# Optimization experiments

Measured on AMD Instinct MI355X. Metric: run time of the kernel, lower is better.

The kernel has to match this reference:

```python
import jax, jax.numpy as jnp
import numpy as np

N_HEADS = 16
D_HEAD = 64
MAX_POS = 128

def setup_inputs() -> dict:
    key = jax.random.key(0)
    ks = jax.random.split(key, 9)
    B, L, D = 4, 1024, 1024
    s = 0.02
    return {
        'x': jax.random.normal(ks[0], (B, L, D), jnp.float32),
        'pad_mask': jnp.ones((B, L), jnp.float32),
        'Wq': jax.random.normal(ks[1], (D, D), jnp.float32) * s,
        'bq': jnp.zeros((D,), jnp.float32),
        'Wk': jax.random.normal(ks[2], (D, D), jnp.float32) * s,
        'bk': jnp.zeros((D,), jnp.float32),
        'Wv': jax.random.normal(ks[3], (D, D), jnp.float32) * s,
        'bv': jnp.zeros((D,), jnp.float32),
        'Wo': jax.random.normal(ks[4], (D, D), jnp.float32) * s,
        'bo': jnp.zeros((D,), jnp.float32),
        'posK': jax.random.normal(ks[5], (2 * MAX_POS + 1, D_HEAD), jnp.float32) * s,
        'posV': jax.random.normal(ks[6], (2 * MAX_POS + 1, D_HEAD), jnp.float32) * s,
    }

def reference(x, pad_mask, Wq, bq, Wk, bk, Wv, bv, Wo, bo, posK, posV):
    B, L, _ = x.shape
    H, d = N_HEADS, D_HEAD
    def proj(W, b):
        y = x @ W + b                      # [B, L, H*d]
        return y.reshape(B, L, H, d).transpose(0, 2, 1, 3)  # [B, H, L, d]
    Q = proj(Wq, bq)
    K = proj(Wk, bk)
    V = proj(Wv, bv)
    # relative position index, clamped to [-MAX_POS, MAX_POS], shifted to [0, 2*MAX_POS]
    idx = jnp.arange(L)
    pos_index = jnp.clip(idx[None, :] - idx[:, None], -MAX_POS, MAX_POS) + MAX_POS  # [L, L]
    pos_emb_K = posK[pos_index]            # [L, L, d]
    pos_emb_V = posV[pos_index]            # [L, L, d]
    S1 = jnp.einsum('bhqd,bhkd->bhqk', Q, K)
    S2 = jnp.einsum('bhqd,qkd->bhqk', Q, pos_emb_K)
    S = (S1 + S2) / np.sqrt(d).astype(np.float32)
    # NOTE: original multiplies scores by the pad mask (not additive -inf)
    S = S * pad_mask[:, None, None, :]
    A = jax.nn.softmax(S, axis=-1)
    O1 = jnp.einsum('bhqk,bhkd->bhqd', A, V)
    O2 = jnp.einsum('bhqk,qkd->bhqd', A, pos_emb_V)
    out = (O1 + O2).transpose(0, 2, 1, 3).reshape(B, L, H * d)
    return out @ Wo + bo
```

## Files before the change

### kernel.cpp

```cpp
#include <hip/hip_runtime.h>
#include <math.h>

#define L_SEQ 1024
#define NB 4
#define NH 16
#define DH 64
#define BH_TOT (NB * NH)
#define GQ_TOT (BH_TOT * L_SEQ)
#define NPOS 257
#define QP_STRIDE 260
#define LDK 72
#define LDQP 68
#define LDPV 264

typedef unsigned short ushort_t;
typedef __attribute__((ext_vector_type(8))) short bf16x8;
typedef __attribute__((ext_vector_type(4))) float f32x4;

__device__ inline ushort_t f2bf_rne(float x) {
    unsigned u = __float_as_uint(x);
    unsigned r = u + 0x7FFFu + ((u >> 16) & 1u);
    return (ushort_t)(r >> 16);
}
__device__ inline float bf2f(ushort_t h) {
    return __uint_as_float(((unsigned)h) << 16);
}
__device__ inline void split8(float4 a0, float4 a1, uint4* H, uint4* L) {
    float v[8] = {a0.x, a0.y, a0.z, a0.w, a1.x, a1.y, a1.z, a1.w};
    unsigned hh[4], ll[4];
    #pragma unroll
    for (int j = 0; j < 4; j++) {
        ushort_t h0 = f2bf_rne(v[2*j]),   h1 = f2bf_rne(v[2*j+1]);
        ushort_t l0 = f2bf_rne(v[2*j]   - bf2f(h0));
        ushort_t l1 = f2bf_rne(v[2*j+1] - bf2f(h1));
        hh[j] = (unsigned)h0 | ((unsigned)h1 << 16);
        ll[j] = (unsigned)l0 | ((unsigned)l1 << 16);
    }
    *H = (uint4){hh[0], hh[1], hh[2], hh[3]};
    *L = (uint4){ll[0], ll[1], ll[2], ll[3]};
}
__device__ inline uint4 pack8hi(float4 a0, float4 a1) {
    float v[8] = {a0.x, a0.y, a0.z, a0.w, a1.x, a1.y, a1.z, a1.w};
    unsigned hh[4];
    #pragma unroll
    for (int j = 0; j < 4; j++)
        hh[j] = (unsigned)f2bf_rne(v[2*j]) | ((unsigned)f2bf_rne(v[2*j+1]) << 16);
    return (uint4){hh[0], hh[1], hh[2], hh[3]};
}

__global__ __launch_bounds__(256)
void split_f32(const float* __restrict__ A, ushort_t* __restrict__ hi,
               ushort_t* __restrict__ lo)
{
    const size_t base = ((size_t)blockIdx.x * 256 + threadIdx.x) * 8;
    uint4 H, L;
    split8(*(const float4*)(A + base), *(const float4*)(A + base + 4), &H, &L);
    *(uint4*)(hi + base) = H;
    *(uint4*)(lo + base) = L;
}

__global__ __launch_bounds__(256)
void split_transpose(const float* __restrict__ W, ushort_t* __restrict__ Thi,
                     ushort_t* __restrict__ Tlo, int Kdim, int Ndim)
{
    __shared__ float Ws[64][65];
    const int tid = threadIdx.x;
    const int k0 = blockIdx.x * 64;
    const int n0 = blockIdx.y * 64;
    const int r  = tid >> 4;
    const int c4 = (tid & 15) * 4;
    #pragma unroll
    for (int i = 0; i < 4; i++) {
        float4 v = *(const float4*)(W + (size_t)(k0 + r + i*16) * Ndim + n0 + c4);
        Ws[r + i*16][c4+0] = v.x;
        Ws[r + i*16][c4+1] = v.y;
        Ws[r + i*16][c4+2] = v.z;
        Ws[r + i*16][c4+3] = v.w;
    }
    __syncthreads();
    #pragma unroll
    for (int i = 0; i < 4; i++) {
        const int nl = r + i*16;
        ushort_t h[4], l[4];
        #pragma unroll
        for (int j = 0; j < 4; j++) {
            float x = Ws[c4 + j][nl];
            h[j] = f2bf_rne(x);
            l[j] = f2bf_rne(x - bf2f(h[j]));
        }
        size_t off = (size_t)(n0 + nl) * Kdim + k0 + c4;
        uint2 H, L;
        H.x = (unsigned)h[0] | ((unsigned)h[1] << 16);
        H.y = (unsigned)h[2] | ((unsigned)h[3] << 16);
        L.x = (unsigned)l[0] | ((unsigned)l[1] << 16);
        L.y = (unsigned)l[2] | ((unsigned)l[3] << 16);
        *(uint2*)(Thi + off) = H;
        *(uint2*)(Tlo + off) = L;
    }
}

__global__ __launch_bounds__(256)
void prep_pvt(const float* __restrict__ posV, ushort_t* __restrict__ pvTg)
{
    __shared__ float Ws[64][65];
    const int tid = threadIdx.x;
    const int c = blockIdx.x;
    {
        const int r  = tid >> 2;
        const int d0 = (tid & 3) * 16;
        const float* src = posV + (size_t)(c * 64 + r + 1) * 64 + d0;
        #pragma unroll
        for (int i = 0; i < 4; i++) {
            float4 v = *(const float4*)(src + i * 4);
            Ws[r][d0 + i*4 + 0] = v.x;
            Ws[r][d0 + i*4 + 1] = v.y;
            Ws[r][d0 + i*4 + 2] = v.z;
            Ws[r][d0 + i*4 + 3] = v.w;
        }
    }
    __syncthreads();
    {
        const int d  = tid >> 2;
        const int r0 = (tid & 3) * 16;
        #pragma unroll
        for (int k = 0; k < 16; k++)
            pvTg[(size_t)d * LDPV + c * 64 + r0 + k] = f2bf_rne(Ws[r0 + k][d]);
    }
}

__global__ __launch_bounds__(256)
void gemm_mfma(const ushort_t* __restrict__ Ahi, const ushort_t* __restrict__ Alo,
               const ushort_t* __restrict__ Bhi, const ushort_t* __restrict__ Blo,
               const float* __restrict__ bias, float* __restrict__ C,
               int M, int N, int K, int mode)
{
    __shared__ ushort_t As[2][64 * LDK];
    __shared__ ushort_t Bs[2][64 * LDK];
    const int tid  = threadIdx.x;
    const int m0   = blockIdx.x * 64;
    const int n0   = blockIdx.y * 64;
    const int wave = tid >> 6;
    const int lane = tid & 63;
    const int w0 = wave >> 1;
    const int w1 = wave & 1;
    const int lr = lane & 15;
    const int lq = lane >> 4;

    f32x4 acc[2][2];
    #pragma unroll
    for (int i = 0; i < 2; i++)
        #pragma unroll
        for (int j = 0; j < 2; j++)
            acc[i][j] = (f32x4){0.f, 0.f, 0.f, 0.f};

    for (int k0 = 0; k0 < K; k0 += 64) {
        __syncthreads();
        #pragma unroll
        for (int c = 0; c < 2; c++) {
            const int n   = c * 256 + tid;
            const int row = n >> 3;
            const int col = (n & 7) * 8;
            const size_t ga = (size_t)(m0 + row) * K + k0 + col;
            const size_t gb = (size_t)(n0 + row) * K + k0 + col;
            const int la = row * LDK + col;
            *(uint4*)&As[0][la] = *(const uint4*)(Ahi + ga);
            *(uint4*)&As[1][la] = *(const uint4*)(Alo + ga);
            *(uint4*)&Bs[0][la] = *(const uint4*)(Bhi + gb);
            *(uint4*)&Bs[1][la] = *(const uint4*)(Blo + gb);
        }
        __syncthreads();
        #pragma unroll
        for (int ks = 0; ks < 2; ks++) {
            bf16x8 ah[2], al[2], bh[2], bl[2];
            #pragma unroll
            for (int i = 0; i < 2; i++) {
                const int ar = (w0*32 + i*16 + lr) * LDK + ks*32 + lq*8;
                ah[i] = *(const bf16x8*)&As[0][ar];
                al[i] = *(const bf16x8*)&As[1][ar];
                const int br = (w1*32 + i*16 + lr) * LDK + ks*32 + lq*8;
                bh[i] = *(const bf16x8*)&Bs[0][br];
                bl[i] = *(const bf16x8*)&Bs[1][br];
            }
            #pragma unroll
            for (int i = 0; i < 2; i++)
                #pragma unroll
                for (int j = 0; j < 2; j++) {
                    acc[i][j] = __builtin_amdgcn_mfma_f32_16x16x32_bf16(ah[i], bh[j], acc[i][j], 0, 0, 0);
                    acc[i][j] = __builtin_amdgcn_mfma_f32_16x16x32_bf16(ah[i], bl[j], acc[i][j], 0, 0, 0);
                    acc[i][j] = __builtin_amdgcn_mfma_f32_16x16x32_bf16(al[i], bh[j], acc[i][j], 0, 0, 0);
                }
        }
    }

    #pragma unroll
    for (int j = 0; j < 2; j++) {
        const int colg = n0 + w1*32 + j*16 + lr;
        const float bcol = bias[colg];
        #pragma unroll
        for (int i = 0; i < 2; i++) {
            #pragma unroll
            for (int r = 0; r < 4; r++) {
                const int m = m0 + w0*32 + i*16 + lq*4 + r;
                const float v = acc[i][j][r] + bcol;
                if (mode == 0) {
                    C[(size_t)m * N + colg] = v;
                } else if (mode == 1) {
                    const int b = m >> 10, lp = m & 1023;
                    const int h = colg >> 6, dd = colg & 63;
                    C[((size_t)(b * NH + h) * L_SEQ + lp) * DH + dd] = v;
                } else {
                    const int b = m >> 10, lp = m & 1023;
                    const int h = colg >> 6, dd = colg & 63;
                    C[((size_t)(b * NH + h) * DH + dd) * L_SEQ + lp] = v;
                }
            }
        }
    }
}

__global__ __launch_bounds__(256)
void qp_kernel(const float* __restrict__ Q, const float* __restrict__ posK,
               ushort_t* __restrict__ Qpu)
{
    __shared__ float Qt[64 * 64];
    __shared__ float Pt[64 * 64];
    const int tid = threadIdx.x;
    const size_t gq0 = (size_t)blockIdx.x * 64;
    const int ty = tid >> 4;
    const int tx = tid & 15;

    {
        const int q  = tid >> 2;
        const int d0 = (tid & 3) * 16;
        const float* qrow = Q + (gq0 + q) * DH + d0;
        #pragma unroll
        for (int i = 0; i < 4; i++) {
            float4 v = *(const float4*)(qrow + i * 4);
            Qt[(d0 + i*4 + 0) * 64 + q] = v.x;
            Qt[(d0 + i*4 + 1) * 64 + q] = v.y;
            Qt[(d0 + i*4 + 2) * 64 + q] = v.z;
            Qt[(d0 + i*4 + 3) * 64 + q] = v.w;
        }
    }

    for (int c = 0; c < 4; c++) {
        __syncthreads();
        {
            const int r  = tid >> 2;
            const int d0 = (tid & 3) * 16;
            const float* krow = posK + (size_t)(c * 64 + r) * DH + d0;
            #pragma unroll
            for (int i = 0; i < 4; i++) {
                float4 v = *(const float4*)(krow + i * 4);
                Pt[(d0 + i*4 + 0) * 64 + r] = v.x;
                Pt[(d0 + i*4 + 1) * 64 + r] = v.y;
                Pt[(d0 + i*4 + 2) * 64 + r] = v.z;
                Pt[(d0 + i*4 + 3) * 64 + r] = v.w;
            }
        }
        __syncthreads();

        float acc[16];
        #pragma unroll
        for (int i = 0; i < 16; i++) acc[i] = 0.f;
        #pragma unroll 16
        for (int d = 0; d < 64; d++) {
            float4 qv = *(const float4*)&Qt[d * 64 + ty * 4];
            float4 pv = *(const float4*)&Pt[d * 64 + tx * 4];
            float qa[4] = {qv.x, qv.y, qv.z, qv.w};
            float pa[4] = {pv.x, pv.y, pv.z, pv.w};
            #pragma unroll
            for (int i = 0; i < 4; i++)
                #pragma unroll
                for (int j = 0; j < 4; j++)
                    acc[i * 4 + j] += qa[i] * pa[j];
        }
        #pragma unroll
        for (int i = 0; i < 4; i++) {
            uint2 o;
            o.x = (unsigned)f2bf_rne(acc[i*4+0]) | ((unsigned)f2bf_rne(acc[i*4+1]) << 16);
            o.y = (unsigned)f2bf_rne(acc[i*4+2]) | ((unsigned)f2bf_rne(acc[i*4+3]) << 16);
            *(uint2*)(Qpu + (gq0 + ty * 4 + i) * QP_STRIDE + c * 64 + tx * 4) = o;
        }
    }

    __syncthreads();
    if (tid < 64) {
        float s = 0.f;
        #pragma unroll 16
        for (int d = 0; d < 64; d++)
            s += Qt[d * 64 + tid] * posK[256 * 64 + d];
        Qpu[(gq0 + tid) * QP_STRIDE + 256] = f2bf_rne(s);
    }
}

__global__ __launch_bounds__(256)
void attn_kernel(const float* __restrict__ Q, const float* __restrict__ K,
                 const float* __restrict__ Vt, const ushort_t* __restrict__ Qpu,
                 const float* __restrict__ pm,
                 ushort_t* __restrict__ SbandU,
                 float* __restrict__ O1a, float* __restrict__ O1b,
                 float* __restrict__ lsum2, float* __restrict__ clo2,
                 float* __restrict__ chi2)
{
    __shared__ ushort_t Qs[64 * LDK];
    __shared__ ushort_t KsPs[64 * LDK];
    __shared__ ushort_t Vs[64 * LDK];
    __shared__ ushort_t Qps[64 * LDQP];
    __shared__ float mk[64];
    __shared__ float redl[128], redc[128], redh[128];

    const int tid = threadIdx.x;
    const int blk = blockIdx.x;
    const int bh  = blk >> 5;
    const int qb  = (blk >> 1) & 15;
    const int ks  = blk & 1;
    const int b   = bh >> 4;
    const int q0  = qb * 64;
    const size_t gq0 = (size_t)bh * L_SEQ + q0;
    const int wave = tid >> 6, lane = tid & 63;
    const int w0 = wave >> 1, w1 = wave & 1;
    const int lr = lane & 15, lq = lane >> 4;

    #pragma unroll
    for (int c = 0; c < 2; c++) {
        const int slot = c * 256 + tid;
        const int row = slot >> 3, col = (slot & 7) * 8;
        const float* src = Q + (gq0 + row) * DH + col;
        *(uint4*)&Qs[row * LDK + col] =
            pack8hi(*(const float4*)src, *(const float4*)(src + 4));
    }

    if (ks == 0 && tid < 64) {
        const int q = q0 + tid;
        ushort_t* bandRow = SbandU + (gq0 + tid) * 256;
        for (int j = 0; j < 127 - q; j++)    bandRow[j] = 0;
        for (int j = 254; j > 1150 - q; j--) bandRow[j] = 0;
        bandRow[255] = 0;
    }

    f32x4 Oacc[2][2];
    #pragma unroll
    for (int i = 0; i < 2; i++)
        #pragma unroll
        for (int j = 0; j < 2; j++)
            Oacc[i][j] = (f32x4){0.f, 0.f, 0.f, 0.f};
    float lpart[2][4] = {}, clpart[2][4] = {}, chpart[2][4] = {};

    const float* Kg  = K  + (size_t)bh * (L_SEQ * DH);
    const float* Vtg = Vt + (size_t)bh * (DH * L_SEQ);

    for (int t = 0; t < 8; t++) {
        const int kt = ks * 8 + t;
        const int k0 = kt * 64;
        __syncthreads();

        #pragma unroll
        for (int c = 0; c < 2; c++) {
            const int slot = c * 256 + tid;
            const int row = slot >> 3, col = (slot & 7) * 8;
            const int la = row * LDK + col;
            const float* ksrc = Kg + (size_t)(k0 + row) * DH + col;
            *(uint4*)&KsPs[la] =
                pack8hi(*(const float4*)ksrc, *(const float4*)(ksrc + 4));
            const float* vsrc = Vtg + (size_t)row * L_SEQ + k0 + col;
            *(uint4*)&Vs[la] =
                pack8hi(*(const float4*)vsrc, *(const float4*)(vsrc + 4));
        }
        #pragma unroll
        for (int tt = 0; tt < 16; tt++) {
            const int idx = tt * 256 + tid;
            const int ql = idx >> 6, kl = idx & 63;
            int rel = k0 + kl - q0 - ql;
            rel = rel < -128 ? -128 : (rel > 128 ? 128 : rel);
            Qps[ql * LDQP + kl] = Qpu[(gq0 + ql) * QP_STRIDE + rel + 128];
        }
        if (tid < 64) mk[tid] = pm[b * L_SEQ + k0 + tid];
        __syncthreads();

        f32x4 Sacc[2][2];
        #pragma unroll
        for (int i = 0; i < 2; i++)
            #pragma unroll
            for (int j = 0; j < 2; j++)
                Sacc[i][j] = (f32x4){0.f, 0.f, 0.f, 0.f};
        #pragma unroll
        for (int kc = 0; kc < 2; kc++) {
            bf16x8 ah[2], bhf[2];
            #pragma unroll
            for (int i = 0; i < 2; i++) {
                ah[i]  = *(const bf16x8*)&Qs[(w0*32 + i*16 + lr) * LDK + kc*32 + lq*8];
                bhf[i] = *(const bf16x8*)&KsPs[(w1*32 + i*16 + lr) * LDK + kc*32 + lq*8];
            }
            #pragma unroll
            for (int i = 0; i < 2; i++)
                #pragma unroll
                for (int j = 0; j < 2; j++)
                    Sacc[i][j] = __builtin_amdgcn_mfma_f32_16x16x32_bf16(ah[i], bhf[j], Sacc[i][j], 0, 0, 0);
        }

        ushort_t pb[2][2][4];
        #pragma unroll
        for (int i = 0; i < 2; i++) {
            #pragma unroll
            for (int r = 0; r < 4; r++) {
                const int ql = w0*32 + i*16 + lq*4 + r;
                const int q  = q0 + ql;
                const size_t gq = gq0 + ql;
                ushort_t* bandRow = SbandU + gq * 256 + 127;
                #pragma unroll
                for (int j = 0; j < 2; j++) {
                    const int kl = w1*32 + j*16 + lr;
                    const int k  = k0 + kl;
                    const int rel = k - q;
                    float s = (Sacc[i][j][r] + bf2f(Qps[ql * LDQP + kl])) * 0.125f;
                    s *= mk[kl];
                    const float p = __expf(s);
                    lpart[i][r] += p;
                    const ushort_t ph = f2bf_rne(p);
                    if (rel <= -128)      clpart[i][r] += p;
                    else if (rel >= 128)  chpart[i][r] += p;
                    else                  bandRow[rel] = ph;
                    pb[i][j][r] = ph;
                }
            }
        }
        __syncthreads();

        #pragma unroll
        for (int i = 0; i < 2; i++)
            #pragma unroll
            for (int j = 0; j < 2; j++)
                #pragma unroll
                for (int r = 0; r < 4; r++) {
                    const int ql = w0*32 + i*16 + lq*4 + r;
                    const int kl = w1*32 + j*16 + lr;
                    KsPs[ql * LDK + kl] = pb[i][j][r];
                }
        __syncthreads();

        #pragma unroll
        for (int kc = 0; kc < 2; kc++) {
            bf16x8 pa[2], vh[2];
            #pragma unroll
            for (int i = 0; i < 2; i++) {
                pa[i] = *(const bf16x8*)&KsPs[(w0*32 + i*16 + lr) * LDK + kc*32 + lq*8];
                vh[i] = *(const bf16x8*)&Vs[(w1*32 + i*16 + lr) * LDK + kc*32 + lq*8];
            }
            #pragma unroll
            for (int i = 0; i < 2; i++)
                #pragma unroll
                for (int j = 0; j < 2; j++)
                    Oacc[i][j] = __builtin_amdgcn_mfma_f32_16x16x32_bf16(pa[i], vh[j], Oacc[i][j], 0, 0, 0);
        }
    }

    #pragma unroll
    for (int off = 1; off < 16; off <<= 1) {
        #pragma unroll
        for (int i = 0; i < 2; i++)
            #pragma unroll
            for (int r = 0; r < 4; r++) {
                lpart[i][r]  += __shfl_xor(lpart[i][r],  off, 64);
                clpart[i][r] += __shfl_xor(clpart[i][r], off, 64);
                chpart[i][r] += __shfl_xor(chpart[i][r], off, 64);
            }
    }
    if (lr == 0) {
        #pragma unroll
        for (int i = 0; i < 2; i++)
            #pragma unroll
            for (int r = 0; r < 4; r++) {
                const int ql = w0*32 + i*16 + lq*4 + r;
                redl[w1 * 64 + ql] = lpart[i][r];
                redc[w1 * 64 + ql] = clpart[i][r];
                redh[w1 * 64 + ql] = chpart[i][r];
            }
    }
    __syncthreads();
    if (tid < 64) {
        const size_t o = (size_t)ks * GQ_TOT + gq0 + tid;
        lsum2[o] = redl[tid] + redl[64 + tid];
        clo2[o]  = redc[tid] + redc[64 + tid];
        chi2[o]  = redh[tid] + redh[64 + tid];
    }

    float* O1o = ks ? O1b : O1a;
    #pragma unroll
    for (int i = 0; i < 2; i++)
        #pragma unroll
        for (int j = 0; j < 2; j++)
            #pragma unroll
            for (int r = 0; r < 4; r++) {
                const int ql = w0*32 + i*16 + lq*4 + r;
                const int dd = w1*32 + j*16 + lr;
                O1o[(gq0 + ql) * DH + dd] = Oacc[i][j][r];
            }
}

__global__ __launch_bounds__(256)
void post_mfma(const ushort_t* __restrict__ SbandU, const ushort_t* __restrict__ pvTg,
               const float* __restrict__ O1a, const float* __restrict__ O1b,
               const float* __restrict__ lsum2, const float* __restrict__ clo2,
               const float* __restrict__ chi2, const float* __restrict__ posV,
               ushort_t* __restrict__ athi, ushort_t* __restrict__ atlo)
{
    __shared__ ushort_t pvT[64 * LDPV];
    const int tid = threadIdx.x;
    const size_t q0 = (size_t)blockIdx.x * 64;
    const int wave = tid >> 6, lane = tid & 63;
    const int w0 = wave >> 1, w1 = wave & 1;
    const int lr = lane & 15, lq = lane >> 4;

    {
        const unsigned* src = (const unsigned*)pvTg;
        unsigned* dst = (unsigned*)pvT;
        for (int i = tid; i < 64 * LDPV / 2; i += 256) dst[i] = src[i];
    }
    __syncthreads();

    f32x4 acc[2][2];
    #pragma unroll
    for (int i = 0; i < 2; i++)
        #pragma unroll
        for (int j = 0; j < 2; j++)
            acc[i][j] = (f32x4){0.f, 0.f, 0.f, 0.f};

    const ushort_t* bandB = SbandU + q0 * 256;
    #pragma unroll
    for (int kc = 0; kc < 8; kc++) {
        bf16x8 a[2], bv[2];
        #pragma unroll
        for (int i = 0; i < 2; i++) {
            a[i]  = *(const bf16x8*)&bandB[(size_t)(w0*32 + i*16 + lr) * 256 + kc*32 + lq*8];
            bv[i] = *(const bf16x8*)&pvT[(w1*32 + i*16 + lr) * LDPV + kc*32 + lq*8];
        }
        #pragma unroll
        for (int i = 0; i < 2; i++)
            #pragma unroll
            for (int j = 0; j < 2; j++)
                acc[i][j] = __builtin_amdgcn_mfma_f32_16x16x32_bf16(a[i], bv[j], acc[i][j], 0, 0, 0);
    }

    #pragma unroll
    for (int i = 0; i < 2; i++) {
        #pragma unroll
        for (int r = 0; r < 4; r++) {
            const int ql = w0*32 + i*16 + lq*4 + r;
            const size_t gq = q0 + ql;
            const float li = lsum2[gq] + lsum2[GQ_TOT + gq];
            const float cl = clo2[gq]  + clo2[GQ_TOT + gq];
            const float ch = chi2[gq]  + chi2[GQ_TOT + gq];
            const float inv = 1.0f / li;
            const int b  = (int)(gq >> 14);
            const int h  = (int)((gq >> 10) & 15);
            const int lp = (int)(gq & 1023);
            const size_t obase = ((size_t)(b * L_SEQ + lp) * 1024) + h * 64;
            #pragma unroll
            for (int j = 0; j < 2; j++) {
                const int dd = w1*32 + j*16 + lr;
                float o = O1a[gq * DH + dd] + O1b[gq * DH + dd] + acc[i][j][r]
                        + cl * posV[dd] + ch * posV[256 * 64 + dd];
                o *= inv;
                const ushort_t hh = f2bf_rne(o);
                const ushort_t ll = f2bf_rne(o - bf2f(hh));
                athi[obase + dd] = hh;
                atlo[obase + dd] = ll;
            }
        }
    }
}

extern "C" void kernel_launch(void* const* d_in, const int* in_sizes, int n_in,
                              void* d_out, int out_size, void* d_ws, size_t ws_size,
                              hipStream_t stream)
{
    const float* x    = (const float*)d_in[0];
    const float* pmk  = (const float*)d_in[1];
    const float* Wq   = (const float*)d_in[2];
    const float* bq   = (const float*)d_in[3];
    const float* Wk   = (const float*)d_in[4];
    const float* bk   = (const float*)d_in[5];
    const float* Wv   = (const float*)d_in[6];
    const float* bv   = (const float*)d_in[7];
    const float* Wo   = (const float*)d_in[8];
    const float* bo   = (const float*)d_in[9];
    const float* posK = (const float*)d_in[10];
    const float* posV = (const float*)d_in[11];
    float* out = (float*)d_out;

    float* ws = (float*)d_ws;
    float* Qb = ws;
    float* Kb = Qb + (size_t)GQ_TOT * DH;
    float* Vb = Kb + (size_t)GQ_TOT * DH;
    ushort_t* Qpu    = (ushort_t*)(Vb + (size_t)GQ_TOT * DH);
    ushort_t* SbandU = Qpu + (size_t)GQ_TOT * QP_STRIDE;
    ushort_t* athi   = SbandU + (size_t)GQ_TOT * 256;
    ushort_t* atlo   = athi + (size_t)GQ_TOT * DH;
    ushort_t* pvTg   = atlo + (size_t)GQ_TOT * DH;
    float* O1a   = (float*)(pvTg + 64 * LDPV);
    float* O1b   = O1a   + (size_t)GQ_TOT * DH;
    float* lsum2 = O1b   + (size_t)GQ_TOT * DH;
    float* clo2  = lsum2 + 2 * (size_t)GQ_TOT;
    float* chi2  = clo2  + 2 * (size_t)GQ_TOT;

    ushort_t* bb  = SbandU;
    ushort_t* xhi = bb;
    ushort_t* xlo = xhi + 4194304;
    ushort_t* wqh = xlo + 4194304;
    ushort_t* wql = wqh + 1048576;
    ushort_t* wkh = wql + 1048576;
    ushort_t* wkl = wkh + 1048576;
    ushort_t* wvh = wkl + 1048576;
    ushort_t* wvl = wvh + 1048576;
    ushort_t* woh = bb;
    ushort_t* wol = woh + 1048576;

    dim3 tg(16, 16), gg(64, 16), gb(256);

    split_f32<<<dim3(2048), gb, 0, stream>>>(x, xhi, xlo);
    split_transpose<<<tg, gb, 0, stream>>>(Wq, wqh, wql, 1024, 1024);
    split_transpose<<<tg, gb, 0, stream>>>(Wk, wkh, wkl, 1024, 1024);
    split_transpose<<<tg, gb, 0, stream>>>(Wv, wvh, wvl, 1024, 1024);
    prep_pvt<<<dim3(4), gb, 0, stream>>>(posV, pvTg);
    gemm_mfma<<<gg, gb, 0, stream>>>(xhi, xlo, wqh, wql, bq, Qb, 4096, 1024, 1024, 1);
    gemm_mfma<<<gg, gb, 0, stream>>>(xhi, xlo, wkh, wkl, bk, Kb, 4096, 1024, 1024, 1);
    gemm_mfma<<<gg, gb, 0, stream>>>(xhi, xlo, wvh, wvl, bv, Vb, 4096, 1024, 1024, 2);
    qp_kernel<<<dim3(GQ_TOT / 64), gb, 0, stream>>>(Qb, posK, Qpu);
    attn_kernel<<<dim3(2048), gb, 0, stream>>>(Qb, Kb, Vb, Qpu, pmk,
                                               SbandU, O1a, O1b, lsum2, clo2, chi2);
    post_mfma<<<dim3(GQ_TOT / 64), gb, 0, stream>>>(SbandU, pvTg, O1a, O1b, lsum2,
                                                    clo2, chi2, posV, athi, atlo);
    split_transpose<<<tg, gb, 0, stream>>>(Wo, woh, wol, 1024, 1024);
    gemm_mfma<<<gg, gb, 0, stream>>>(athi, atlo, woh, wol, bo, out, 4096, 1024, 1024, 0);
}
```

Baseline: 439.6 us.

## Restructure attention kernel: per-wave query rows, register Q, prefetch next K/V tile

```diff
diff --git a/kernel.cpp b/kernel.cpp
--- a/kernel.cpp
+++ b/kernel.cpp
@@ -10,7 +10,7 @@
 #define NPOS 257
 #define QP_STRIDE 260
 #define LDK 72
-#define LDQP 68
+#define LDQP 72
 #define LDPV 264
 
 typedef unsigned short ushort_t;
@@ -303,12 +303,10 @@
                  float* __restrict__ lsum2, float* __restrict__ clo2,
                  float* __restrict__ chi2)
 {
-    __shared__ ushort_t Qs[64 * LDK];
-    __shared__ ushort_t KsPs[64 * LDK];
+    __shared__ ushort_t Ks[64 * LDK];
     __shared__ ushort_t Vs[64 * LDK];
-    __shared__ ushort_t Qps[64 * LDQP];
+    __shared__ ushort_t QpsP[64 * LDQP];
     __shared__ float mk[64];
-    __shared__ float redl[128], redc[128], redh[128];
 
     const int tid = threadIdx.x;
     const int blk = blockIdx.x;
@@ -319,16 +317,26 @@
     const int q0  = qb * 64;
     const size_t gq0 = (size_t)bh * L_SEQ + q0;
     const int wave = tid >> 6, lane = tid & 63;
-    const int w0 = wave >> 1, w1 = wave & 1;
     const int lr = lane & 15, lq = lane >> 4;
-
-    #pragma unroll
-    for (int c = 0; c < 2; c++) {
-        const int slot = c * 256 + tid;
-        const int row = slot >> 3, col = (slot & 7) * 8;
-        const float* src = Q + (gq0 + row) * DH + col;
-        *(uint4*)&Qs[row * LDK + col] =
-            pack8hi(*(const float4*)src, *(const float4*)(src + 4));
+    const int qw = wave * 16;
+
+    const int sr0 = tid >> 3,          sc0 = (tid & 7) * 8;
+    const int sr1 = (256 + tid) >> 3,  sc1 = ((256 + tid) & 7) * 8;
+    const int qpRowL = qw + (lane >> 2);
+    const int qpCol0 = (lane & 3) * 16;
+
+    const float* Kg  = K  + (size_t)bh * (L_SEQ * DH);
+    const float* Vtg = Vt + (size_t)bh * (DH * L_SEQ);
+
+    bf16x8 qa[2];
+    {
+        const float* qrow = Q + (gq0 + qw + lr) * DH;
+        #pragma unroll
+        for (int kc = 0; kc < 2; kc++) {
+            const float* s = qrow + kc * 32 + lq * 8;
+            uint4 u = pack8hi(*(const float4*)s, *(const float4*)(s + 4));
+            qa[kc] = *(bf16x8*)&u;
+        }
     }
 
     if (ks == 0 && tid < 64) {
@@ -339,163 +347,149 @@
         bandRow[255] = 0;
     }
 
-    f32x4 Oacc[2][2];
-    #pragma unroll
-    for (int i = 0; i < 2; i++)
-        #pragma unroll
-        for (int j = 0; j < 2; j++)
-            Oacc[i][j] = (f32x4){0.f, 0.f, 0.f, 0.f};
-    float lpart[2][4] = {}, clpart[2][4] = {}, chpart[2][4] = {};
-
-    const float* Kg  = K  + (size_t)bh * (L_SEQ * DH);
-    const float* Vtg = Vt + (size_t)bh * (DH * L_SEQ);
+    f32x4 Oacc[4];
+    #pragma unroll
+    for (int j = 0; j < 4; j++) Oacc[j] = (f32x4){0.f, 0.f, 0.f, 0.f};
+    float lpart[4] = {}, clpart[4] = {}, chpart[4] = {};
+
+    float4 kva[2][2], kvb[2][2];
+    ushort_t qpr[16];
+    float mkr = 0.f;
+    {
+        const int k0 = ks * 512;
+        const float* ka0 = Kg + (size_t)(k0 + sr0) * DH + sc0;
+        const float* ka1 = Kg + (size_t)(k0 + sr1) * DH + sc1;
+        kva[0][0] = *(const float4*)ka0;      kva[0][1] = *(const float4*)(ka0 + 4);
+        kva[1][0] = *(const float4*)ka1;      kva[1][1] = *(const float4*)(ka1 + 4);
+        const float* va0 = Vtg + (size_t)sr0 * L_SEQ + k0 + sc0;
+        const float* va1 = Vtg + (size_t)sr1 * L_SEQ + k0 + sc1;
+        kvb[0][0] = *(const float4*)va0;      kvb[0][1] = *(const float4*)(va0 + 4);
+        kvb[1][0] = *(const float4*)va1;      kvb[1][1] = *(const float4*)(va1 + 4);
+        const int qg = q0 + qpRowL;
+        #pragma unroll
+        for (int c = 0; c < 16; c++) {
+            int rel = k0 + qpCol0 + c - qg;
+            rel = rel < -128 ? -128 : (rel > 128 ? 128 : rel);
+            qpr[c] = Qpu[(gq0 + qpRowL) * QP_STRIDE + rel + 128];
+        }
+        if (tid < 64) mkr = pm[b * L_SEQ + k0 + tid];
+    }
 
     for (int t = 0; t < 8; t++) {
-        const int kt = ks * 8 + t;
-        const int k0 = kt * 64;
+        const int k0 = (ks * 8 + t) * 64;
         __syncthreads();
 
-        #pragma unroll
-        for (int c = 0; c < 2; c++) {
-            const int slot = c * 256 + tid;
-            const int row = slot >> 3, col = (slot & 7) * 8;
-            const int la = row * LDK + col;
-            const float* ksrc = Kg + (size_t)(k0 + row) * DH + col;
-            *(uint4*)&KsPs[la] =
-                pack8hi(*(const float4*)ksrc, *(const float4*)(ksrc + 4));
-            const float* vsrc = Vtg + (size_t)row * L_SEQ + k0 + col;
-            *(uint4*)&Vs[la] =
-                pack8hi(*(const float4*)vsrc, *(const float4*)(vsrc + 4));
-        }
-        #pragma unroll
-        for (int tt = 0; tt < 16; tt++) {
-            const int idx = tt * 256 + tid;
-            const int ql = idx >> 6, kl = idx & 63;
-            int rel = k0 + kl - q0 - ql;
-            rel = rel < -128 ? -128 : (rel > 128 ? 128 : rel);
-            Qps[ql * LDQP + kl] = Qpu[(gq0 + ql) * QP_STRIDE + rel + 128];
-        }
-        if (tid < 64) mk[tid] = pm[b * L_SEQ + k0 + tid];
+        *(uint4*)&Ks[sr0 * LDK + sc0] = pack8hi(kva[0][0], kva[0][1]);
+        *(uint4*)&Ks[sr1 * LDK + sc1] = pack8hi(kva[1][0], kva[1][1]);
+        *(uint4*)&Vs[sr0 * LDK + sc0] = pack8hi(kvb[0][0], kvb[0][1]);
+        *(uint4*)&Vs[sr1 * LDK + sc1] = pack8hi(kvb[1][0], kvb[1][1]);
+        {
+            ushort_t* dst = &QpsP[qpRowL * LDQP + qpCol0];
+            #pragma unroll
+            for (int c = 0; c < 8; c++)
+                ((unsigned*)dst)[c] = (unsigned)qpr[2*c] | ((unsigned)qpr[2*c+1] << 16);
+        }
+        if (tid < 64) mk[tid] = mkr;
         __syncthreads();
 
-        f32x4 Sacc[2][2];
-        #pragma unroll
-        for (int i = 0; i < 2; i++)
-            #pragma unroll
-            for (int j = 0; j < 2; j++)
-                Sacc[i][j] = (f32x4){0.f, 0.f, 0.f, 0.f};
+        if (t < 7) {
+            const int k0n = k0 + 64;
+            const float* ka0 = Kg + (size_t)(k0n + sr0) * DH + sc0;
+            const float* ka1 = Kg + (size_t)(k0n + sr1) * DH + sc1;
+            kva[0][0] = *(const float4*)ka0;  kva[0][1] = *(const float4*)(ka0 + 4);
+            kva[1][0] = *(const float4*)ka1;  kva[1][1] = *(const float4*)(ka1 + 4);
+            const float* va0 = Vtg + (size_t)sr0 * L_SEQ + k0n + sc0;
+            const float* va1 = Vtg + (size_t)sr1 * L_SEQ + k0n + sc1;
+            kvb[0][0] = *(const float4*)va0;  kvb[0][1] = *(const float4*)(va0 + 4);
+            kvb[1][0] = *(const float4*)va1;  kvb[1][1] = *(const float4*)(va1 + 4);
+            const int qg = q0 + qpRowL;
+            #pragma unroll
+            for (int c = 0; c < 16; c++) {
+                int rel = k0n + qpCol0 + c - qg;
+                rel = rel < -128 ? -128 : (rel > 128 ? 128 : rel);
+                qpr[c] = Qpu[(gq0 + qpRowL) * QP_STRIDE + rel + 128];
+            }
+            if (tid < 64) mkr = pm[b * L_SEQ + k0n + tid];
+        }
+
+        f32x4 Sacc[4];
+        #pragma unroll
+        for (int j = 0; j < 4; j++) Sacc[j] = (f32x4){0.f, 0.f, 0.f, 0.f};
         #pragma unroll
         for (int kc = 0; kc < 2; kc++) {
-            bf16x8 ah[2], bhf[2];
-            #pragma unroll
-            for (int i = 0; i < 2; i++) {
-                ah[i]  = *(const bf16x8*)&Qs[(w0*32 + i*16 + lr) * LDK + kc*32 + lq*8];
-                bhf[i] = *(const bf16x8*)&KsPs[(w1*32 + i*16 + lr) * LDK + kc*32 + lq*8];
-            }
-            #pragma unroll
-            for (int i = 0; i < 2; i++)
-                #pragma unroll
-                for (int j = 0; j < 2; j++)
-                    Sacc[i][j] = __builtin_amdgcn_mfma_f32_16x16x32_bf16(ah[i], bhf[j], Sacc[i][j], 0, 0, 0);
-        }
-
-        ushort_t pb[2][2][4];
-        #pragma unroll
-        for (int i = 0; i < 2; i++) {
-            #pragma unroll
-            for (int r = 0; r < 4; r++) {
-                const int ql = w0*32 + i*16 + lq*4 + r;
-                const int q  = q0 + ql;
-                const size_t gq = gq0 + ql;
-                ushort_t* bandRow = SbandU + gq * 256 + 127;
-                #pragma unroll
-                for (int j = 0; j < 2; j++) {
-                    const int kl = w1*32 + j*16 + lr;
-                    const int k  = k0 + kl;
-                    const int rel = k - q;
-                    float s = (Sacc[i][j][r] + bf2f(Qps[ql * LDQP + kl])) * 0.125f;
-                    s *= mk[kl];
-                    const float p = __expf(s);
-                    lpart[i][r] += p;
-                    const ushort_t ph = f2bf_rne(p);
-                    if (rel <= -128)      clpart[i][r] += p;
-                    else if (rel >= 128)  chpart[i][r] += p;
-                    else                  bandRow[rel] = ph;
-                    pb[i][j][r] = ph;
-                }
-            }
-        }
-        __syncthreads();
-
-        #pragma unroll
-        for (int i = 0; i < 2; i++)
-            #pragma unroll
-            for (int j = 0; j < 2; j++)
-                #pragma unroll
-                for (int r = 0; r < 4; r++) {
-                    const int ql = w0*32 + i*16 + lq*4 + r;
-                    const int kl = w1*32 + j*16 + lr;
-                    KsPs[ql * LDK + kl] = pb[i][j][r];
-                }
-        __syncthreads();
+            #pragma unroll
+            for (int j = 0; j < 4; j++) {
+                bf16x8 kb = *(const bf16x8*)&Ks[(j*16 + lr) * LDK + kc*32 + lq*8];
+                Sacc[j] = __builtin_amdgcn_mfma_f32_16x16x32_bf16(qa[kc], kb, Sacc[j], 0, 0, 0);
+            }
+        }
+
+        ushort_t pb[4][4];
+        #pragma unroll
+        for (int r = 0; r < 4; r++) {
+            const int ql = qw + lq*4 + r;
+            const int q  = q0 + ql;
+            const size_t gq = gq0 + ql;
+            ushort_t* bandRow = SbandU + gq * 256 + 127;
+            #pragma unroll
+            for (int j = 0; j < 4; j++) {
+                const int kl = j*16 + lr;
+                const int k  = k0 + kl;
+                const int rel = k - q;
+                float s = (Sacc[j][r] + bf2f(QpsP[ql * LDQP + kl])) * 0.125f;
+                s *= mk[kl];
+                const float p = __expf(s);
+                lpart[r] += p;
+                const ushort_t ph = f2bf_rne(p);
+                if (rel <= -128)      clpart[r] += p;
+                else if (rel >= 128)  chpart[r] += p;
+                else                  bandRow[rel] = ph;
+                pb[j][r] = ph;
+            }
+        }
+
+        #pragma unroll
+        for (int r = 0; r < 4; r++)
+            #pragma unroll
+            for (int j = 0; j < 4; j++)
+                QpsP[(qw + lq*4 + r) * LDQP + j*16 + lr] = pb[j][r];
 
         #pragma unroll
         for (int kc = 0; kc < 2; kc++) {
-            bf16x8 pa[2], vh[2];
-            #pragma unroll
-            for (int i = 0; i < 2; i++) {
-                pa[i] = *(const bf16x8*)&KsPs[(w0*32 + i*16 + lr) * LDK + kc*32 + lq*8];
-                vh[i] = *(const bf16x8*)&Vs[(w1*32 + i*16 + lr) * LDK + kc*32 + lq*8];
-            }
-            #pragma unroll
-            for (int i = 0; i < 2; i++)
-                #pragma unroll
-                for (int j = 0; j < 2; j++)
-                    Oacc[i][j] = __builtin_amdgcn_mfma_f32_16x16x32_bf16(pa[i], vh[j], Oacc[i][j], 0, 0, 0);
+            bf16x8 pa = *(const bf16x8*)&QpsP[(qw + lr) * LDQP + kc*32 + lq*8];
+            #pragma unroll
+            for (int j = 0; j < 4; j++) {
+                bf16x8 vb = *(const bf16x8*)&Vs[(j*16 + lr) * LDK + kc*32 + lq*8];
+                Oacc[j] = __builtin_amdgcn_mfma_f32_16x16x32_bf16(pa, vb, Oacc[j], 0, 0, 0);
+            }
         }
     }
 
     #pragma unroll
     for (int off = 1; off < 16; off <<= 1) {
         #pragma unroll
-        for (int i = 0; i < 2; i++)
-            #pragma unroll
-            for (int r = 0; r < 4; r++) {
-                lpart[i][r]  += __shfl_xor(lpart[i][r],  off, 64);
-                clpart[i][r] += __shfl_xor(clpart[i][r], off, 64);
-                chpart[i][r] += __shfl_xor(chpart[i][r], off, 64);
-            }
+        for (int r = 0; r < 4; r++) {
+            lpart[r]  += __shfl_xor(lpart[r],  off, 64);
+            clpart[r] += __shfl_xor(clpart[r], off, 64);
+            chpart[r] += __shfl_xor(chpart[r], off, 64);
+        }
     }
     if (lr == 0) {
         #pragma unroll
-        for (int i = 0; i < 2; i++)
-            #pragma unroll
-            for (int r = 0; r < 4; r++) {
-                const int ql = w0*32 + i*16 + lq*4 + r;
-                redl[w1 * 64 + ql] = lpart[i][r];
-                redc[w1 * 64 + ql] = clpart[i][r];
-                redh[w1 * 64 + ql] = chpart[i][r];
-            }
-    }
-    __syncthreads();
-    if (tid < 64) {
-        const size_t o = (size_t)ks * GQ_TOT + gq0 + tid;
-        lsum2[o] = redl[tid] + redl[64 + tid];
-        clo2[o]  = redc[tid] + redc[64 + tid];
-        chi2[o]  = redh[tid] + redh[64 + tid];
+        for (int r = 0; r < 4; r++) {
+            const size_t o = (size_t)ks * GQ_TOT + gq0 + qw + lq*4 + r;
+            lsum2[o] = lpart[r];
+            clo2[o]  = clpart[r];
+            chi2[o]  = chpart[r];
+        }
     }
 
     float* O1o = ks ? O1b : O1a;
     #pragma unroll
-    for (int i = 0; i < 2; i++)
-        #pragma unroll
-        for (int j = 0; j < 2; j++)
-            #pragma unroll
-            for (int r = 0; r < 4; r++) {
-                const int ql = w0*32 + i*16 + lq*4 + r;
-                const int dd = w1*32 + j*16 + lr;
-                O1o[(gq0 + ql) * DH + dd] = Oacc[i][j][r];
-            }
+    for (int j = 0; j < 4; j++)
+        #pragma unroll
+        for (int r = 0; r < 4; r++)
+            O1o[(gq0 + qw + lq*4 + r) * DH + j*16 + lr] = Oacc[j][r];
 }
 
 __global__ __launch_bounds__(256)
```

Measured after the change: 447.4 us. About the same (+1.8%).
